# Optimization experiments

Hardware: AMD Instinct MI355X
Metric: run time of the kernel (lower is better)

Reference implementation:

```python
import jax, jax.numpy as jnp
import numpy as np

B, N, D, H, E = 4, 2048, 512, 8, 64  # batch, seq, model dim, heads, head dim
EPS = 1e-6
PAD = -2.0
NEG_INF = -1000000000.0
ROPE_MAX = 2048
ROPE_BASE = 10000.0


def compute_rope_rotations(dim, max_seq_len, base):
    inv_freq = 1.0 / base ** (jnp.arange(0, dim, 2, dtype=jnp.float32) / dim)
    pos = jnp.arange(max_seq_len, dtype=jnp.float32)
    freqs = pos[:, None] * inv_freq[None, :]          # (L, dim/2)
    freqs = jnp.repeat(freqs, 2, axis=-1)             # (L, dim)
    return jnp.cos(freqs), jnp.sin(freqs)


def apply_rope(x, cos, sin):
    # Faithful to the source: positions are indexed along AXIS 1 of x.
    # Since q/k have layout (b, h, n, e), axis 1 is the HEAD axis (source quirk).
    seq = x.shape[1]
    c = cos[:seq][None, :, None, :]
    s = sin[:seq][None, :, None, :]
    x1, x2 = x[..., 0::2], x[..., 1::2]
    ch, sh = c[..., 0::2], s[..., 0::2]
    r1 = x1 * ch - x2 * sh
    r2 = x1 * sh + x2 * ch
    return jnp.stack([r1, r2], axis=-1).reshape(x.shape)


def layer_norm(x, gamma, beta):
    mean = jnp.mean(x, axis=-1, keepdims=True)
    var = jnp.mean(jnp.square(x - mean), axis=-1, keepdims=True)
    return gamma * ((x - mean) / jnp.sqrt(var + EPS)) + beta


def setup_inputs() -> dict:
    key = jax.random.key(0)
    ks = jax.random.split(key, 10)
    x = jax.random.normal(ks[0], (B, N, D), dtype=jnp.float32)
    mask = jnp.where(jax.random.uniform(ks[1], (B, N)) < 0.1, PAD, 1.0).astype(jnp.float32)
    glorot_qkv = float(np.sqrt(6.0 / (D + E)))
    q_proj = jax.random.uniform(ks[2], (H, D, E), minval=-glorot_qkv, maxval=glorot_qkv, dtype=jnp.float32)
    k_proj = jax.random.uniform(ks[3], (H, D, E), minval=-glorot_qkv, maxval=glorot_qkv, dtype=jnp.float32)
    v_proj = jax.random.uniform(ks[4], (H, D, E), minval=-glorot_qkv, maxval=glorot_qkv, dtype=jnp.float32)
    g = jax.random.uniform(ks[5], (H, D, E), minval=-0.05, maxval=0.05, dtype=jnp.float32)
    glorot_out = float(np.sqrt(6.0 / (H * E + D)))
    out_w = jax.random.uniform(ks[6], (H * E, D), minval=-glorot_out, maxval=glorot_out, dtype=jnp.float32)
    out_b = jnp.zeros((D,), dtype=jnp.float32)
    gamma_in = jnp.ones((D,), dtype=jnp.float32)
    beta_in = jnp.zeros((D,), dtype=jnp.float32)
    gamma_out = jnp.ones((D,), dtype=jnp.float32)
    beta_out = jnp.zeros((D,), dtype=jnp.float32)
    rope_cos, rope_sin = compute_rope_rotations(E, ROPE_MAX, ROPE_BASE)
    return dict(x=x, mask=mask, q_proj=q_proj, k_proj=k_proj, v_proj=v_proj, g=g,
                gamma_in=gamma_in, beta_in=beta_in, gamma_out=gamma_out, beta_out=beta_out,
                out_w=out_w, out_b=out_b, rope_cos=rope_cos, rope_sin=rope_sin)


def reference(x, mask, q_proj, k_proj, v_proj, g, gamma_in, beta_in,
              gamma_out, beta_out, out_w, out_b, rope_cos, rope_sin):
    scale = 1.0 / jnp.sqrt(jnp.asarray(E, dtype=x.dtype))
    q_input = layer_norm(x, gamma_in, beta_in)          # self-attention: shared LN input
    mask_bin = jnp.where(mask == PAD, 0.0, 1.0).astype(x.dtype)  # (B, N)
    q = jnp.einsum('bnd,hde->bhne', q_input, q_proj)
    k = jnp.einsum('bmd,hde->bhme', q_input, k_proj)
    v = jnp.einsum('bmd,hde->bhme', q_input, v_proj)
    q = apply_rope(q, rope_cos, rope_sin)
    k = apply_rope(k, rope_cos, rope_sin)
    att = jnp.einsum('bhne,bhme->bhnm', q, k) * scale   # (B, H, N, N)
    amask = mask_bin[:, None, :, None] * mask_bin[:, None, None, :]  # (B,1,N,N)
    att = att + (1.0 - amask) * NEG_INF
    att = jax.nn.softmax(att, axis=-1) * amask
    out = jnp.einsum('bhnm,bhme->bhne', att, v)
    gate = jax.nn.sigmoid(jnp.einsum('bnd,hde->bhne', q_input, g))
    out = out * gate
    out = out.transpose(0, 2, 1, 3).reshape(x.shape[0], x.shape[1], H * E)
    out = out @ out_w + out_b
    out = out + x  # residual
    return layer_norm(out, gamma_out, beta_out)


if __name__ == '__main__':
    inp = setup_inputs()
    y = reference(**inp)
    print(y.shape, y.dtype)
```

## Files before the change

kernel.cpp:

```cpp
#include <hip/hip_runtime.h>
#include <math.h>

#define B_ 4
#define N_ 2048
#define D_ 512
#define H_ 8
#define E_ 64

constexpr float EPS = 1e-6f;
constexpr float PADV = -2.0f;
constexpr float SCALE = 0.125f;

typedef __attribute__((ext_vector_type(8))) __bf16 bf16x8;
typedef __attribute__((ext_vector_type(4))) float f32x4;
typedef __attribute__((ext_vector_type(8))) unsigned short u16x8;

__device__ inline unsigned short f2bf(float f) {
  unsigned u = __builtin_bit_cast(unsigned, f);
  u += 0x7fffu + ((u >> 16) & 1u);
  return (unsigned short)(u >> 16);
}
__device__ inline float bf2f(unsigned short v) {
  unsigned u = ((unsigned)v) << 16;
  return __builtin_bit_cast(float, u);
}

__global__ __launch_bounds__(256) void prep_kernel(
    const float* __restrict__ qp, const float* __restrict__ kp,
    const float* __restrict__ vp, const float* __restrict__ gp,
    const float* __restrict__ ow, ushort* __restrict__ wT,
    ushort* __restrict__ owT) {
  __shared__ float Ls[64][65];
  int t = threadIdx.x;
  const float* src;
  ushort* dst;
  int src_ld, r0, c0;
  if (blockIdx.x < 256) {
    int set = blockIdx.x >> 6, tile = blockIdx.x & 63;
    int h = tile >> 3, dt = tile & 7;
    const float* w = set == 0 ? qp : set == 1 ? kp : set == 2 ? vp : gp;
    src = w + (size_t)h * 512 * 64;
    src_ld = 64;
    r0 = dt * 64;
    c0 = 0;
    dst = wT + ((size_t)set * 512 + h * 64) * 512;
  } else {
    int idx = blockIdx.x - 256;
    src = ow;
    src_ld = 512;
    r0 = (idx >> 3) * 64;
    c0 = (idx & 7) * 64;
    dst = owT;
  }
#pragma unroll
  for (int i = 0; i < 4; i++) {
    int id = t + i * 256;
    int r = id >> 4, c4 = (id & 15) * 4;
    float4 v = *(const float4*)(src + (size_t)(r0 + r) * src_ld + c0 + c4);
    Ls[r][c4] = v.x;
    Ls[r][c4 + 1] = v.y;
    Ls[r][c4 + 2] = v.z;
    Ls[r][c4 + 3] = v.w;
  }
  __syncthreads();
#pragma unroll
  for (int i = 0; i < 4; i++) {
    int id = t + i * 256;
    int c = id >> 4, r4 = (id & 15) * 4;
    ushort4 o;
    o.x = f2bf(Ls[r4][c]);
    o.y = f2bf(Ls[r4 + 1][c]);
    o.z = f2bf(Ls[r4 + 2][c]);
    o.w = f2bf(Ls[r4 + 3][c]);
    *(ushort4*)(dst + (size_t)(c0 + c) * 512 + r0 + r4) = o;
  }
}

__global__ __launch_bounds__(256) void ln_bf16_kernel(
    const float* __restrict__ x, const float* __restrict__ gamma,
    const float* __restrict__ beta, ushort* __restrict__ out) {
  int row = blockIdx.x;
  const float* xr = x + (size_t)row * D_;
  int c0 = threadIdx.x, c1 = threadIdx.x + 256;
  float v0 = xr[c0], v1 = xr[c1];

  __shared__ float red[8];
  int lane = threadIdx.x & 63, wid = threadIdx.x >> 6;

  float s = v0 + v1;
  for (int o = 32; o > 0; o >>= 1) s += __shfl_down(s, o, 64);
  if (lane == 0) red[wid] = s;
  __syncthreads();
  float mean = (red[0] + red[1] + red[2] + red[3]) * (1.0f / D_);

  float d0 = v0 - mean, d1 = v1 - mean;
  float sq = d0 * d0 + d1 * d1;
  for (int o = 32; o > 0; o >>= 1) sq += __shfl_down(sq, o, 64);
  if (lane == 0) red[4 + wid] = sq;
  __syncthreads();
  float var = (red[4] + red[5] + red[6] + red[7]) * (1.0f / D_);
  float rstd = rsqrtf(var + EPS);

  ushort* orow = out + (size_t)row * D_;
  orow[c0] = f2bf(gamma[c0] * (d0 * rstd) + beta[c0]);
  orow[c1] = f2bf(gamma[c1] * (d1 * rstd) + beta[c1]);
}

__global__ __launch_bounds__(256) void ln_kernel(
    const float* __restrict__ x, const float* __restrict__ gamma,
    const float* __restrict__ beta, float* __restrict__ out) {
  int row = blockIdx.x;
  const float* xr = x + (size_t)row * D_;
  int c0 = threadIdx.x, c1 = threadIdx.x + 256;
  float v0 = xr[c0], v1 = xr[c1];

  __shared__ float red[8];
  int lane = threadIdx.x & 63, wid = threadIdx.x >> 6;

  float s = v0 + v1;
  for (int o = 32; o > 0; o >>= 1) s += __shfl_down(s, o, 64);
  if (lane == 0) red[wid] = s;
  __syncthreads();
  float mean = (red[0] + red[1] + red[2] + red[3]) * (1.0f / D_);

  float d0 = v0 - mean, d1 = v1 - mean;
  float sq = d0 * d0 + d1 * d1;
  for (int o = 32; o > 0; o >>= 1) sq += __shfl_down(sq, o, 64);
  if (lane == 0) red[4 + wid] = sq;
  __syncthreads();
  float var = (red[4] + red[5] + red[6] + red[7]) * (1.0f / D_);
  float rstd = rsqrtf(var + EPS);

  float* orow = out + (size_t)row * D_;
  orow[c0] = gamma[c0] * (d0 * rstd) + beta[c0];
  orow[c1] = gamma[c1] * (d1 * rstd) + beta[c1];
}

__global__ __launch_bounds__(256) void proj_kernel(
    const ushort* __restrict__ xbf, const ushort* __restrict__ wT,
    const float* __restrict__ rope_cos, const float* __restrict__ rope_sin,
    ushort* __restrict__ qo, ushort* __restrict__ ko,
    ushort* __restrict__ vTo, ushort* __restrict__ go) {
  int tileM = blockIdx.x;
  int h = blockIdx.y & 7;
  int set = blockIdx.y >> 3;

  __shared__ ushort As[128 * 64];
  __shared__ ushort Bs[64 * 64];

  const int t = threadIdx.x;
  const int w = t >> 6;
  const int lane = t & 63;
  const int quad = lane >> 4;
  const int n15 = lane & 15;

  const ushort* wbase = wT + ((size_t)set * 512 + h * 64) * 512;
  const int bn0 = tileM * 128;

  f32x4 acc[2][4];
#pragma unroll
  for (int mb = 0; mb < 2; mb++)
#pragma unroll
    for (int tt = 0; tt < 4; tt++) acc[mb][tt] = (f32x4){0.f, 0.f, 0.f, 0.f};

  for (int k0 = 0; k0 < 512; k0 += 64) {
    __syncthreads();
#pragma unroll
    for (int i = 0; i < 4; i++) {
      int c = t + i * 256;
      int row = c >> 3, c8 = c & 7;
      *(uint4*)&As[(row << 6) + ((c8 ^ (row & 7)) << 3)] =
          *(const uint4*)(xbf + (size_t)(bn0 + row) * 512 + k0 + (c8 << 3));
    }
#pragma unroll
    for (int i = 0; i < 2; i++) {
      int c = t + i * 256;
      int row = c >> 3, c8 = c & 7;
      *(uint4*)&Bs[(row << 6) + ((c8 ^ (row & 7)) << 3)] =
          *(const uint4*)(wbase + (size_t)row * 512 + k0 + (c8 << 3));
    }
    __syncthreads();
#pragma unroll
    for (int kk = 0; kk < 2; kk++) {
      bf16x8 af[2], bfr[4];
#pragma unroll
      for (int mb = 0; mb < 2; mb++) {
        int m = 32 * w + 16 * mb + n15;
        af[mb] = __builtin_bit_cast(
            bf16x8,
            *(const uint4*)&As[(m << 6) + ((((kk << 2) + quad) ^ (m & 7)) << 3)]);
      }
#pragma unroll
      for (int tt = 0; tt < 4; tt++) {
        int n = 16 * tt + n15;
        bfr[tt] = __builtin_bit_cast(
            bf16x8,
            *(const uint4*)&Bs[(n << 6) + ((((kk << 2) + quad) ^ (n & 7)) << 3)]);
      }
#pragma unroll
      for (int mb = 0; mb < 2; mb++)
#pragma unroll
        for (int tt = 0; tt < 4; tt++)
          acc[mb][tt] = __builtin_amdgcn_mfma_f32_16x16x32_bf16(
              af[mb], bfr[tt], acc[mb][tt], 0, 0, 0);
    }
  }

  const int b = bn0 >> 11;
  const int n_base = bn0 & 2047;
  const int bh = b * H_ + h;
  const size_t bhN = (size_t)bh * N_;

  if (set <= 1) {
    ushort* dst = (set == 0) ? qo : ko;
    const float sgn = (n15 & 1) ? 1.f : -1.f;
#pragma unroll
    for (int tt = 0; tt < 4; tt++) {
      int e = 16 * tt + n15;
      float cv = rope_cos[(h << 6) + e];
      float sv = rope_sin[(h << 6) + e];
#pragma unroll
      for (int mb = 0; mb < 2; mb++) {
#pragma unroll
        for (int r = 0; r < 4; r++) {
          float xv = acc[mb][tt][r];
          float pv = __shfl_xor(xv, 1, 64);
          float ov = xv * cv + sgn * pv * sv;
          int n = n_base + 32 * w + 16 * mb + 4 * quad + r;
          dst[((bhN + n) << 6) + e] = f2bf(ov);
        }
      }
    }
  } else if (set == 2) {
#pragma unroll
    for (int tt = 0; tt < 4; tt++) {
      int e = 16 * tt + n15;
#pragma unroll
      for (int mb = 0; mb < 2; mb++) {
        int n0 = n_base + 32 * w + 16 * mb + 4 * quad;
        ushort4 pk;
        pk.x = f2bf(acc[mb][tt][0]);
        pk.y = f2bf(acc[mb][tt][1]);
        pk.z = f2bf(acc[mb][tt][2]);
        pk.w = f2bf(acc[mb][tt][3]);
        *(ushort4*)(vTo + ((size_t)(bh * 64 + e)) * N_ + n0) = pk;
      }
    }
  } else {
#pragma unroll
    for (int tt = 0; tt < 4; tt++) {
      int e = 16 * tt + n15;
#pragma unroll
      for (int mb = 0; mb < 2; mb++) {
#pragma unroll
        for (int r = 0; r < 4; r++) {
          int n = n_base + 32 * w + 16 * mb + 4 * quad + r;
          float sv = 1.0f / (1.0f + __expf(-acc[mb][tt][r]));
          go[((bhN + n) << 6) + e] = f2bf(sv);
        }
      }
    }
  }
}

__global__ __launch_bounds__(256) void attn_kernel(
    const ushort* __restrict__ qb, const ushort* __restrict__ kb,
    const ushort* __restrict__ vT, const ushort* __restrict__ gb,
    const float* __restrict__ mask, ushort* __restrict__ out) {
  int qt = blockIdx.x;
  int bh = blockIdx.y;
  int b = bh >> 3, h = bh & 7;

  __shared__ ushort Ks[64 * 64];
  __shared__ ushort Vts[64 * 64];
  __shared__ ushort Pt[64 * 66];
  __shared__ float km[64];

  const int t = threadIdx.x;
  const int w = t >> 6;
  const int lane = t & 63;
  const int quad = lane >> 4;
  const int n15 = lane & 15;

  const size_t bhN = (size_t)bh * N_;
  const size_t bN = (size_t)b * N_;
  const int qt64 = qt * 64;

  const ushort* qrow = qb + ((bhN + qt64 + 16 * w + n15) << 6);
  bf16x8 qf0 = __builtin_bit_cast(bf16x8, *(const uint4*)(qrow + (quad << 3)));
  bf16x8 qf1 =
      __builtin_bit_cast(bf16x8, *(const uint4*)(qrow + 32 + (quad << 3)));

  f32x4 O[4];
  float m_i[4], l_i[4];
#pragma unroll
  for (int i = 0; i < 4; i++) {
    O[i] = (f32x4){0.f, 0.f, 0.f, 0.f};
    m_i[i] = -1e9f;
    l_i[i] = 0.f;
  }

  for (int m0 = 0; m0 < N_; m0 += 64) {
    __syncthreads();
#pragma unroll
    for (int i = 0; i < 2; i++) {
      int c = t + i * 256;
      int row = c >> 3, col8 = c & 7;
      int loff = (row << 6) + ((col8 ^ (row & 7)) << 3);
      *(uint4*)(&Ks[loff]) =
          *(const uint4*)(kb + ((bhN + m0 + row) << 6) + (col8 << 3));
      *(uint4*)(&Vts[loff]) =
          *(const uint4*)(vT + (size_t)(bh * 64 + row) * N_ + m0 + (col8 << 3));
    }
    if (t < 64) km[t] = (mask[bN + m0 + t] == PADV) ? 0.f : 1.f;
    __syncthreads();

    f32x4 st[4];
#pragma unroll
    for (int tt = 0; tt < 4; tt++) st[tt] = (f32x4){0.f, 0.f, 0.f, 0.f};
#pragma unroll
    for (int tt = 0; tt < 4; tt++) {
      int rbase = (tt * 16 + n15) << 6;
      bf16x8 k0 = __builtin_bit_cast(
          bf16x8, *(const uint4*)(&Ks[rbase + ((quad ^ (n15 & 7)) << 3)]));
      bf16x8 k1 = __builtin_bit_cast(
          bf16x8,
          *(const uint4*)(&Ks[rbase + (((4 + quad) ^ (n15 & 7)) << 3)]));
      st[tt] = __builtin_amdgcn_mfma_f32_16x16x32_bf16(qf0, k0, st[tt], 0, 0, 0);
      st[tt] = __builtin_amdgcn_mfma_f32_16x16x32_bf16(qf1, k1, st[tt], 0, 0, 0);
    }

    float kmv[4];
#pragma unroll
    for (int tt = 0; tt < 4; tt++) kmv[tt] = km[tt * 16 + n15];
#pragma unroll
    for (int tt = 0; tt < 4; tt++) {
      bool live = (kmv[tt] != 0.f);
#pragma unroll
      for (int r = 0; r < 4; r++)
        st[tt][r] = live ? st[tt][r] * SCALE : -1e9f;
    }

    float alpha[4];
#pragma unroll
    for (int r = 0; r < 4; r++) {
      float mx = fmaxf(fmaxf(st[0][r], st[1][r]), fmaxf(st[2][r], st[3][r]));
#pragma unroll
      for (int o = 1; o < 16; o <<= 1) mx = fmaxf(mx, __shfl_xor(mx, o, 64));
      float mn = fmaxf(m_i[r], mx);
      alpha[r] = __expf(m_i[r] - mn);
      m_i[r] = mn;
      float rs = 0.f;
#pragma unroll
      for (int tt = 0; tt < 4; tt++) {
        float p = __expf(st[tt][r] - mn);
        st[tt][r] = p;
        rs += p;
      }
#pragma unroll
      for (int o = 1; o < 16; o <<= 1) rs += __shfl_xor(rs, o, 64);
      l_i[r] = l_i[r] * alpha[r] + rs;
    }

#pragma unroll
    for (int tt = 0; tt < 4; tt++) {
      int kbase = (tt * 16 + n15) * 66 + 16 * w + 4 * quad;
#pragma unroll
      for (int p = 0; p < 2; p++) {
        ushort2 pk2;
        pk2.x = f2bf(st[tt][2 * p]);
        pk2.y = f2bf(st[tt][2 * p + 1]);
        *(ushort2*)(&Pt[kbase + 2 * p]) = pk2;
      }
    }
#pragma unroll
    for (int tt = 0; tt < 4; tt++)
#pragma unroll
      for (int r = 0; r < 4; r++) O[tt][r] *= alpha[r];

    __syncthreads();

    bf16x8 pf0, pf1;
    {
      u16x8 a, c;
#pragma unroll
      for (int j = 0; j < 8; j++) {
        a[j] = Pt[(quad * 8 + j) * 66 + 16 * w + n15];
        c[j] = Pt[(32 + quad * 8 + j) * 66 + 16 * w + n15];
      }
      pf0 = __builtin_bit_cast(bf16x8, a);
      pf1 = __builtin_bit_cast(bf16x8, c);
    }
#pragma unroll
    for (int tt = 0; tt < 4; tt++) {
      int rbase = (tt * 16 + n15) << 6;
      bf16x8 v0 = __builtin_bit_cast(
          bf16x8, *(const uint4*)(&Vts[rbase + ((quad ^ (n15 & 7)) << 3)]));
      bf16x8 v1 = __builtin_bit_cast(
          bf16x8,
          *(const uint4*)(&Vts[rbase + (((4 + quad) ^ (n15 & 7)) << 3)]));
      O[tt] = __builtin_amdgcn_mfma_f32_16x16x32_bf16(pf0, v0, O[tt], 0, 0, 0);
      O[tt] = __builtin_amdgcn_mfma_f32_16x16x32_bf16(pf1, v1, O[tt], 0, 0, 0);
    }
  }

#pragma unroll
  for (int r = 0; r < 4; r++) {
    int n = qt64 + 16 * w + 4 * quad + r;
    float qm = (mask[bN + n] == PADV) ? 0.f : 1.f;
    float inv = qm / l_i[r];
    const ushort* grow = gb + ((bhN + n) << 6);
    ushort* orow = out + ((bN + n) << 9) + (h << 6);
#pragma unroll
    for (int tt = 0; tt < 4; tt++) {
      int e = tt * 16 + n15;
      orow[e] = f2bf(O[tt][r] * inv * bf2f(grow[e]));
    }
  }
}

__global__ __launch_bounds__(256) void outproj_kernel(
    const ushort* __restrict__ ain, const ushort* __restrict__ owT,
    const float* __restrict__ bias, const float* __restrict__ xres,
    float* __restrict__ out) {
  int tileM = blockIdx.x;
  int cc0 = blockIdx.y * 64;

  __shared__ ushort As[128 * 64];
  __shared__ ushort Bs[64 * 64];

  const int t = threadIdx.x;
  const int w = t >> 6;
  const int lane = t & 63;
  const int quad = lane >> 4;
  const int n15 = lane & 15;

  const ushort* wbase = owT + (size_t)cc0 * 512;
  const int bn0 = tileM * 128;

  f32x4 acc[2][4];
#pragma unroll
  for (int mb = 0; mb < 2; mb++)
#pragma unroll
    for (int tt = 0; tt < 4; tt++) acc[mb][tt] = (f32x4){0.f, 0.f, 0.f, 0.f};

  for (int k0 = 0; k0 < 512; k0 += 64) {
    __syncthreads();
#pragma unroll
    for (int i = 0; i < 4; i++) {
      int c = t + i * 256;
      int row = c >> 3, c8 = c & 7;
      *(uint4*)&As[(row << 6) + ((c8 ^ (row & 7)) << 3)] =
          *(const uint4*)(ain + (size_t)(bn0 + row) * 512 + k0 + (c8 << 3));
    }
#pragma unroll
    for (int i = 0; i < 2; i++) {
      int c = t + i * 256;
      int row = c >> 3, c8 = c & 7;
      *(uint4*)&Bs[(row << 6) + ((c8 ^ (row & 7)) << 3)] =
          *(const uint4*)(wbase + (size_t)row * 512 + k0 + (c8 << 3));
    }
    __syncthreads();
#pragma unroll
    for (int kk = 0; kk < 2; kk++) {
      bf16x8 af[2], bfr[4];
#pragma unroll
      for (int mb = 0; mb < 2; mb++) {
        int m = 32 * w + 16 * mb + n15;
        af[mb] = __builtin_bit_cast(
            bf16x8,
            *(const uint4*)&As[(m << 6) + ((((kk << 2) + quad) ^ (m & 7)) << 3)]);
      }
#pragma unroll
      for (int tt = 0; tt < 4; tt++) {
        int n = 16 * tt + n15;
        bfr[tt] = __builtin_bit_cast(
            bf16x8,
            *(const uint4*)&Bs[(n << 6) + ((((kk << 2) + quad) ^ (n & 7)) << 3)]);
      }
#pragma unroll
      for (int mb = 0; mb < 2; mb++)
#pragma unroll
        for (int tt = 0; tt < 4; tt++)
          acc[mb][tt] = __builtin_amdgcn_mfma_f32_16x16x32_bf16(
              af[mb], bfr[tt], acc[mb][tt], 0, 0, 0);
    }
  }

#pragma unroll
  for (int tt = 0; tt < 4; tt++) {
    int c = cc0 + 16 * tt + n15;
    float bv = bias[c];
#pragma unroll
    for (int mb = 0; mb < 2; mb++) {
#pragma unroll
      for (int r = 0; r < 4; r++) {
        size_t row = bn0 + 32 * w + 16 * mb + 4 * quad + r;
        out[row * 512 + c] = acc[mb][tt][r] + bv + xres[row * 512 + c];
      }
    }
  }
}

extern "C" void kernel_launch(void* const* d_in, const int* in_sizes, int n_in,
                              void* d_out, int out_size, void* d_ws,
                              size_t ws_size, hipStream_t stream) {
  (void)in_sizes; (void)n_in; (void)out_size; (void)ws_size;
  const float* x = (const float*)d_in[0];
  const float* mask = (const float*)d_in[1];
  const float* q_proj = (const float*)d_in[2];
  const float* k_proj = (const float*)d_in[3];
  const float* v_proj = (const float*)d_in[4];
  const float* g = (const float*)d_in[5];
  const float* gamma_in = (const float*)d_in[6];
  const float* beta_in = (const float*)d_in[7];
  const float* gamma_out = (const float*)d_in[8];
  const float* beta_out = (const float*)d_in[9];
  const float* out_w = (const float*)d_in[10];
  const float* out_b = (const float*)d_in[11];
  const float* rope_cos = (const float*)d_in[12];
  const float* rope_sin = (const float*)d_in[13];

  char* p = (char*)d_ws;
  ushort* xbf   = (ushort*)p; p += (size_t)8 << 20;
  ushort* wT    = (ushort*)p; p += (size_t)2 << 20;
  ushort* owT   = (ushort*)p; p += (size_t)1 << 20;
  ushort* qb16  = (ushort*)p; p += (size_t)8 << 20;
  ushort* kb16  = (ushort*)p; p += (size_t)8 << 20;
  ushort* vT16  = (ushort*)p; p += (size_t)8 << 20;
  ushort* gate  = (ushort*)p; p += (size_t)8 << 20;
  ushort* attnb = (ushort*)p; p += (size_t)8 << 20;
  float* ypre   = (float*)p;  p += (size_t)16 << 20;

  prep_kernel<<<320, 256, 0, stream>>>(q_proj, k_proj, v_proj, g, out_w, wT,
                                       owT);

  ln_bf16_kernel<<<B_ * N_, 256, 0, stream>>>(x, gamma_in, beta_in, xbf);

  dim3 gp(64, 32);
  proj_kernel<<<gp, 256, 0, stream>>>(xbf, wT, rope_cos, rope_sin, qb16, kb16,
                                      vT16, gate);

  dim3 ga(32, 32);
  attn_kernel<<<ga, 256, 0, stream>>>(qb16, kb16, vT16, gate, mask, attnb);

  dim3 go(64, 8);
  outproj_kernel<<<go, 256, 0, stream>>>(attnb, owT, out_b, x, ypre);

  ln_kernel<<<B_ * N_, 256, 0, stream>>>(ypre, gamma_out, beta_out,
                                         (float*)d_out);
}
```

Baseline: 267.1 us.

## Restructure attention kernel: 128-row query tiles, transposed S, exp2, MFMA row sums

Each block now handles 128 query rows, and each wave owns 32 of them, so every K/V tile loaded into shared memory is reused twice as much. The grid halves to match. S is computed transposed, with K as the A operand, so each wave writes P into its own shared buffer, which removes the second block-wide barrier per iteration. The softmax scale and log2(e) are folded into Q during projection so exp2 can replace exp, and the key mask becomes an additive bias. Row sums come from an extra MFMA against a row of bf16 ones rather than shuffle reductions. This raises register pressure and halves the number of blocks, which may cut occupancy, and P is rounded by a simple add without round-to-nearest-even.

Result: faster. 253.0 us (-5.3%).

```diff
diff --git a/kernel.cpp b/kernel.cpp
--- a/kernel.cpp
+++ b/kernel.cpp
@@ -9,11 +9,10 @@
 
 constexpr float EPS = 1e-6f;
 constexpr float PADV = -2.0f;
-constexpr float SCALE = 0.125f;
+constexpr float SCL = 0.18033688011112043f;
 
 typedef __attribute__((ext_vector_type(8))) __bf16 bf16x8;
 typedef __attribute__((ext_vector_type(4))) float f32x4;
-typedef __attribute__((ext_vector_type(8))) unsigned short u16x8;
 
 __device__ inline unsigned short f2bf(float f) {
   unsigned u = __builtin_bit_cast(unsigned, f);
@@ -83,16 +82,13 @@
   const float* xr = x + (size_t)row * D_;
   int c0 = threadIdx.x, c1 = threadIdx.x + 256;
   float v0 = xr[c0], v1 = xr[c1];
-
   __shared__ float red[8];
   int lane = threadIdx.x & 63, wid = threadIdx.x >> 6;
-
   float s = v0 + v1;
   for (int o = 32; o > 0; o >>= 1) s += __shfl_down(s, o, 64);
   if (lane == 0) red[wid] = s;
   __syncthreads();
   float mean = (red[0] + red[1] + red[2] + red[3]) * (1.0f / D_);
-
   float d0 = v0 - mean, d1 = v1 - mean;
   float sq = d0 * d0 + d1 * d1;
   for (int o = 32; o > 0; o >>= 1) sq += __shfl_down(sq, o, 64);
@@ -100,7 +96,6 @@
   __syncthreads();
   float var = (red[4] + red[5] + red[6] + red[7]) * (1.0f / D_);
   float rstd = rsqrtf(var + EPS);
-
   ushort* orow = out + (size_t)row * D_;
   orow[c0] = f2bf(gamma[c0] * (d0 * rstd) + beta[c0]);
   orow[c1] = f2bf(gamma[c1] * (d1 * rstd) + beta[c1]);
@@ -113,16 +108,13 @@
   const float* xr = x + (size_t)row * D_;
   int c0 = threadIdx.x, c1 = threadIdx.x + 256;
   float v0 = xr[c0], v1 = xr[c1];
-
   __shared__ float red[8];
   int lane = threadIdx.x & 63, wid = threadIdx.x >> 6;
-
   float s = v0 + v1;
   for (int o = 32; o > 0; o >>= 1) s += __shfl_down(s, o, 64);
   if (lane == 0) red[wid] = s;
   __syncthreads();
   float mean = (red[0] + red[1] + red[2] + red[3]) * (1.0f / D_);
-
   float d0 = v0 - mean, d1 = v1 - mean;
   float sq = d0 * d0 + d1 * d1;
   for (int o = 32; o > 0; o >>= 1) sq += __shfl_down(sq, o, 64);
@@ -130,7 +122,6 @@
   __syncthreads();
   float var = (red[4] + red[5] + red[6] + red[7]) * (1.0f / D_);
   float rstd = rsqrtf(var + EPS);
-
   float* orow = out + (size_t)row * D_;
   orow[c0] = gamma[c0] * (d0 * rstd) + beta[c0];
   orow[c1] = gamma[c1] * (d1 * rstd) + beta[c1];
@@ -213,6 +204,7 @@
 
   if (set <= 1) {
     ushort* dst = (set == 0) ? qo : ko;
+    const float oscale = (set == 0) ? SCL : 1.0f;
     const float sgn = (n15 & 1) ? 1.f : -1.f;
 #pragma unroll
     for (int tt = 0; tt < 4; tt++) {
@@ -225,7 +217,7 @@
         for (int r = 0; r < 4; r++) {
           float xv = acc[mb][tt][r];
           float pv = __shfl_xor(xv, 1, 64);
-          float ov = xv * cv + sgn * pv * sv;
+          float ov = (xv * cv + sgn * pv * sv) * oscale;
           int n = n_base + 32 * w + 16 * mb + 4 * quad + r;
           dst[((bhN + n) << 6) + e] = f2bf(ov);
         }
@@ -271,150 +263,170 @@
   int bh = blockIdx.y;
   int b = bh >> 3, h = bh & 7;
 
-  __shared__ ushort Ks[64 * 64];
-  __shared__ ushort Vts[64 * 64];
-  __shared__ ushort Pt[64 * 66];
-  __shared__ float km[64];
+  __shared__ uint Ksu[64 * 32];
+  __shared__ uint Vtsu[66 * 32];
+  __shared__ uint Pw[4 * 32 * 36];
+  __shared__ __align__(16) float kmb[64];
 
   const int t = threadIdx.x;
   const int w = t >> 6;
   const int lane = t & 63;
   const int quad = lane >> 4;
   const int n15 = lane & 15;
+  const int sw = n15 & 7;
 
   const size_t bhN = (size_t)bh * N_;
   const size_t bN = (size_t)b * N_;
-  const int qt64 = qt * 64;
-
-  const ushort* qrow = qb + ((bhN + qt64 + 16 * w + n15) << 6);
-  bf16x8 qf0 = __builtin_bit_cast(bf16x8, *(const uint4*)(qrow + (quad << 3)));
-  bf16x8 qf1 =
-      __builtin_bit_cast(bf16x8, *(const uint4*)(qrow + 32 + (quad << 3)));
-
-  f32x4 O[4];
-  float m_i[4], l_i[4];
-#pragma unroll
-  for (int i = 0; i < 4; i++) {
-    O[i] = (f32x4){0.f, 0.f, 0.f, 0.f};
-    m_i[i] = -1e9f;
-    l_i[i] = 0.f;
-  }
+  const int q0 = qt * 128 + 32 * w;
+
+  bf16x8 qf[2][2];
+#pragma unroll
+  for (int mb = 0; mb < 2; mb++) {
+    const ushort* qrow = qb + ((bhN + q0 + 16 * mb + n15) << 6);
+#pragma unroll
+    for (int hf = 0; hf < 2; hf++)
+      qf[mb][hf] =
+          __builtin_bit_cast(bf16x8, *(const uint4*)(qrow + 32 * hf + (quad << 3)));
+  }
+
+  if (t < 32) Vtsu[64 * 32 + t] = 0x3f803f80u;
+
+  f32x4 O[2][4], O5[2];
+  float m_i[2];
+#pragma unroll
+  for (int mb = 0; mb < 2; mb++) {
+    m_i[mb] = -1e9f;
+    O5[mb] = (f32x4){0.f, 0.f, 0.f, 0.f};
+#pragma unroll
+    for (int tt = 0; tt < 4; tt++) O[mb][tt] = (f32x4){0.f, 0.f, 0.f, 0.f};
+  }
+
+  uint* Pq = &Pw[w * 1152];
 
   for (int m0 = 0; m0 < N_; m0 += 64) {
     __syncthreads();
 #pragma unroll
     for (int i = 0; i < 2; i++) {
-      int c = t + i * 256;
-      int row = c >> 3, col8 = c & 7;
-      int loff = (row << 6) + ((col8 ^ (row & 7)) << 3);
-      *(uint4*)(&Ks[loff]) =
-          *(const uint4*)(kb + ((bhN + m0 + row) << 6) + (col8 << 3));
-      *(uint4*)(&Vts[loff]) =
-          *(const uint4*)(vT + (size_t)(bh * 64 + row) * N_ + m0 + (col8 << 3));
-    }
-    if (t < 64) km[t] = (mask[bN + m0 + t] == PADV) ? 0.f : 1.f;
+      int u = t + i * 256;
+      int row = u >> 3, c8 = u & 7;
+      int dst = row * 32 + ((c8 ^ (row & 7)) << 2);
+      *(uint4*)&Ksu[dst] =
+          *(const uint4*)(kb + ((bhN + m0 + row) << 6) + (c8 << 3));
+      *(uint4*)&Vtsu[dst] =
+          *(const uint4*)(vT + (size_t)(bh * 64 + row) * N_ + m0 + (c8 << 3));
+    }
+    if (t < 16) {
+      f32x4 mv = *(const f32x4*)(mask + bN + m0 + 4 * t);
+      f32x4 bias;
+#pragma unroll
+      for (int j = 0; j < 4; j++) bias[j] = (mv[j] == PADV) ? -1e9f : 0.f;
+      *(f32x4*)&kmb[4 * t] = bias;
+    }
     __syncthreads();
 
-    f32x4 st[4];
-#pragma unroll
-    for (int tt = 0; tt < 4; tt++) st[tt] = (f32x4){0.f, 0.f, 0.f, 0.f};
-#pragma unroll
-    for (int tt = 0; tt < 4; tt++) {
-      int rbase = (tt * 16 + n15) << 6;
-      bf16x8 k0 = __builtin_bit_cast(
-          bf16x8, *(const uint4*)(&Ks[rbase + ((quad ^ (n15 & 7)) << 3)]));
-      bf16x8 k1 = __builtin_bit_cast(
-          bf16x8,
-          *(const uint4*)(&Ks[rbase + (((4 + quad) ^ (n15 & 7)) << 3)]));
-      st[tt] = __builtin_amdgcn_mfma_f32_16x16x32_bf16(qf0, k0, st[tt], 0, 0, 0);
-      st[tt] = __builtin_amdgcn_mfma_f32_16x16x32_bf16(qf1, k1, st[tt], 0, 0, 0);
-    }
-
-    float kmv[4];
-#pragma unroll
-    for (int tt = 0; tt < 4; tt++) kmv[tt] = km[tt * 16 + n15];
-#pragma unroll
-    for (int tt = 0; tt < 4; tt++) {
-      bool live = (kmv[tt] != 0.f);
-#pragma unroll
-      for (int r = 0; r < 4; r++)
-        st[tt][r] = live ? st[tt][r] * SCALE : -1e9f;
-    }
-
-    float alpha[4];
+    f32x4 st[2][4];
+#pragma unroll
+    for (int mb = 0; mb < 2; mb++)
+#pragma unroll
+      for (int tt = 0; tt < 4; tt++) st[mb][tt] = (f32x4){0.f, 0.f, 0.f, 0.f};
+#pragma unroll
+    for (int hf = 0; hf < 2; hf++) {
+#pragma unroll
+      for (int tt = 0; tt < 4; tt++) {
+        bf16x8 kf = __builtin_bit_cast(
+            bf16x8, *(const uint4*)&Ksu[(16 * tt + n15) * 32 +
+                                        (((quad + 4 * hf) ^ sw) << 2)]);
+        st[0][tt] =
+            __builtin_amdgcn_mfma_f32_16x16x32_bf16(kf, qf[0][hf], st[0][tt], 0, 0, 0);
+        st[1][tt] =
+            __builtin_amdgcn_mfma_f32_16x16x32_bf16(kf, qf[1][hf], st[1][tt], 0, 0, 0);
+      }
+    }
+
+    f32x4 bias[4];
+#pragma unroll
+    for (int tt = 0; tt < 4; tt++)
+      bias[tt] = *(const f32x4*)&kmb[16 * tt + 4 * quad];
+
+#pragma unroll
+    for (int mb = 0; mb < 2; mb++) {
+#pragma unroll
+      for (int tt = 0; tt < 4; tt++) st[mb][tt] += bias[tt];
+      float mx = -1e30f;
+#pragma unroll
+      for (int tt = 0; tt < 4; tt++)
+#pragma unroll
+        for (int r = 0; r < 4; r++) mx = fmaxf(mx, st[mb][tt][r]);
+      mx = fmaxf(mx, __shfl_xor(mx, 16, 64));
+      mx = fmaxf(mx, __shfl_xor(mx, 32, 64));
+      float mn = fmaxf(m_i[mb], mx);
+      float al = __builtin_exp2f(m_i[mb] - mn);
+      m_i[mb] = mn;
+
+      int rowb = (16 * mb + n15) * 36;
+#pragma unroll
+      for (int tt = 0; tt < 4; tt++) {
+        uint u0 = __builtin_bit_cast(uint, __builtin_exp2f(st[mb][tt][0] - mn)) + 0x8000u;
+        uint u1 = __builtin_bit_cast(uint, __builtin_exp2f(st[mb][tt][1] - mn)) + 0x8000u;
+        uint u2 = __builtin_bit_cast(uint, __builtin_exp2f(st[mb][tt][2] - mn)) + 0x8000u;
+        uint u3 = __builtin_bit_cast(uint, __builtin_exp2f(st[mb][tt][3] - mn)) + 0x8000u;
+        int c8p = (2 * tt + (quad >> 1)) ^ sw;
+        int a = rowb + (c8p << 2) + ((quad & 1) << 1);
+        Pq[a] = __builtin_amdgcn_perm(u1, u0, 0x07060302u);
+        Pq[a + 1] = __builtin_amdgcn_perm(u3, u2, 0x07060302u);
+      }
+
+      float alo[4];
+#pragma unroll
+      for (int r = 0; r < 4; r++) alo[r] = __shfl(al, 4 * quad + r, 64);
+#pragma unroll
+      for (int tt = 0; tt < 4; tt++)
+#pragma unroll
+        for (int r = 0; r < 4; r++) O[mb][tt][r] *= alo[r];
+#pragma unroll
+      for (int r = 0; r < 4; r++) O5[mb][r] *= alo[r];
+    }
+    __asm__ volatile("" ::: "memory");
+
+#pragma unroll
+    for (int hf = 0; hf < 2; hf++) {
+      bf16x8 pf[2];
+#pragma unroll
+      for (int mb = 0; mb < 2; mb++)
+        pf[mb] = __builtin_bit_cast(
+            bf16x8, *(const uint4*)&Pq[(16 * mb + n15) * 36 +
+                                       (((quad + 4 * hf) ^ sw) << 2)]);
+      bf16x8 lf = __builtin_bit_cast(
+          bf16x8, *(const uint4*)&Vtsu[64 * 32 + ((quad + 4 * hf) << 2)]);
+      O5[0] = __builtin_amdgcn_mfma_f32_16x16x32_bf16(pf[0], lf, O5[0], 0, 0, 0);
+      O5[1] = __builtin_amdgcn_mfma_f32_16x16x32_bf16(pf[1], lf, O5[1], 0, 0, 0);
+#pragma unroll
+      for (int tt = 0; tt < 4; tt++) {
+        bf16x8 vf = __builtin_bit_cast(
+            bf16x8, *(const uint4*)&Vtsu[(16 * tt + n15) * 32 +
+                                         (((quad + 4 * hf) ^ sw) << 2)]);
+        O[0][tt] =
+            __builtin_amdgcn_mfma_f32_16x16x32_bf16(pf[0], vf, O[0][tt], 0, 0, 0);
+        O[1][tt] =
+            __builtin_amdgcn_mfma_f32_16x16x32_bf16(pf[1], vf, O[1][tt], 0, 0, 0);
+      }
+    }
+  }
+
+#pragma unroll
+  for (int mb = 0; mb < 2; mb++) {
 #pragma unroll
     for (int r = 0; r < 4; r++) {
-      float mx = fmaxf(fmaxf(st[0][r], st[1][r]), fmaxf(st[2][r], st[3][r]));
-#pragma unroll
-      for (int o = 1; o < 16; o <<= 1) mx = fmaxf(mx, __shfl_xor(mx, o, 64));
-      float mn = fmaxf(m_i[r], mx);
-      alpha[r] = __expf(m_i[r] - mn);
-      m_i[r] = mn;
-      float rs = 0.f;
+      int n = q0 + 16 * mb + 4 * quad + r;
+      float qm = (mask[bN + n] == PADV) ? 0.f : 1.f;
+      float inv = qm / fmaxf(O5[mb][r], 1e-30f);
+      const ushort* grow = gb + ((bhN + n) << 6);
+      ushort* orow = out + ((bN + n) << 9) + (h << 6);
 #pragma unroll
       for (int tt = 0; tt < 4; tt++) {
-        float p = __expf(st[tt][r] - mn);
-        st[tt][r] = p;
-        rs += p;
-      }
-#pragma unroll
-      for (int o = 1; o < 16; o <<= 1) rs += __shfl_xor(rs, o, 64);
-      l_i[r] = l_i[r] * alpha[r] + rs;
-    }
-
-#pragma unroll
-    for (int tt = 0; tt < 4; tt++) {
-      int kbase = (tt * 16 + n15) * 66 + 16 * w + 4 * quad;
-#pragma unroll
-      for (int p = 0; p < 2; p++) {
-        ushort2 pk2;
-        pk2.x = f2bf(st[tt][2 * p]);
-        pk2.y = f2bf(st[tt][2 * p + 1]);
-        *(ushort2*)(&Pt[kbase + 2 * p]) = pk2;
-      }
-    }
-#pragma unroll
-    for (int tt = 0; tt < 4; tt++)
-#pragma unroll
-      for (int r = 0; r < 4; r++) O[tt][r] *= alpha[r];
-
-    __syncthreads();
-
-    bf16x8 pf0, pf1;
-    {
-      u16x8 a, c;
-#pragma unroll
-      for (int j = 0; j < 8; j++) {
-        a[j] = Pt[(quad * 8 + j) * 66 + 16 * w + n15];
-        c[j] = Pt[(32 + quad * 8 + j) * 66 + 16 * w + n15];
-      }
-      pf0 = __builtin_bit_cast(bf16x8, a);
-      pf1 = __builtin_bit_cast(bf16x8, c);
-    }
-#pragma unroll
-    for (int tt = 0; tt < 4; tt++) {
-      int rbase = (tt * 16 + n15) << 6;
-      bf16x8 v0 = __builtin_bit_cast(
-          bf16x8, *(const uint4*)(&Vts[rbase + ((quad ^ (n15 & 7)) << 3)]));
-      bf16x8 v1 = __builtin_bit_cast(
-          bf16x8,
-          *(const uint4*)(&Vts[rbase + (((4 + quad) ^ (n15 & 7)) << 3)]));
-      O[tt] = __builtin_amdgcn_mfma_f32_16x16x32_bf16(pf0, v0, O[tt], 0, 0, 0);
-      O[tt] = __builtin_amdgcn_mfma_f32_16x16x32_bf16(pf1, v1, O[tt], 0, 0, 0);
-    }
-  }
-
-#pragma unroll
-  for (int r = 0; r < 4; r++) {
-    int n = qt64 + 16 * w + 4 * quad + r;
-    float qm = (mask[bN + n] == PADV) ? 0.f : 1.f;
-    float inv = qm / l_i[r];
-    const ushort* grow = gb + ((bhN + n) << 6);
-    ushort* orow = out + ((bN + n) << 9) + (h << 6);
-#pragma unroll
-    for (int tt = 0; tt < 4; tt++) {
-      int e = tt * 16 + n15;
-      orow[e] = f2bf(O[tt][r] * inv * bf2f(grow[e]));
+        int e = 16 * tt + n15;
+        orow[e] = f2bf(O[mb][tt][r] * inv * bf2f(grow[e]));
+      }
     }
   }
 }
@@ -541,7 +553,7 @@
   proj_kernel<<<gp, 256, 0, stream>>>(xbf, wT, rope_cos, rope_sin, qb16, kb16,
                                       vT16, gate);
 
-  dim3 ga(32, 32);
+  dim3 ga(16, 32);
   attn_kernel<<<ga, 256, 0, stream>>>(qb16, kb16, vT16, gate, mask, attnb);
 
   dim3 go(64, 8);
```
